# Kernel tuning notes

Hardware: AMD Instinct MI355X
Metric: run time of the kernel (lower is better)

Reference implementation:

```python
import jax, jax.numpy as jnp
import numpy as np

B = 64        # number of graphs
NPG = 4096    # nodes per graph (equal-size segments, batch ids sorted)
H = 256       # hidden_dim
C0, C1 = 256, 64  # num_clusters


def setup_inputs() -> dict:
    key = jax.random.key(0)
    ks = jax.random.split(key, 8)
    N = B * NPG
    x = jax.random.normal(ks[0], (N, H), dtype=jnp.float32)
    edge_index = jax.random.randint(ks[1], (2, N), 0, N, dtype=jnp.int64)  # unused by forward
    batch = jnp.repeat(jnp.arange(B, dtype=jnp.int64), NPG)  # sorted, equal-size segments
    s = 1.0 / np.sqrt(H)
    W0 = jax.random.uniform(ks[2], (H, C0), jnp.float32, -s, s)
    b0 = jax.random.uniform(ks[3], (C0,), jnp.float32, -s, s)
    W1 = jax.random.uniform(ks[4], (H, C1), jnp.float32, -s, s)
    b1 = jax.random.uniform(ks[5], (C1,), jnp.float32, -s, s)
    sf = 1.0 / np.sqrt(C1 * H)
    Wf = jax.random.uniform(ks[6], (C1 * H, H), jnp.float32, -sf, sf)
    bf = jax.random.uniform(ks[7], (H,), jnp.float32, -sf, sf)
    return {"x": x, "edge_index": edge_index, "batch": batch,
            "W0": W0, "b0": b0, "W1": W1, "b1": b1, "Wf": Wf, "bf": bf}


def reference(x, edge_index, batch, W0, b0, W1, b1, Wf, bf):
    # Level 0: softmax cluster assignment + per-graph segmented matmul A^T @ F.
    # batch ids are sorted with equal-size segments, so the per-graph Python
    # loop of the original collapses to a reshape + batched einsum.
    A0 = jax.nn.softmax(x @ W0 + b0, axis=-1)                      # [N, C0]
    f0 = jnp.einsum('bnc,bnh->bch',
                    A0.reshape(B, NPG, C0),
                    x.reshape(B, NPG, H)).reshape(B * C0, H)        # [B*C0, H]
    # Level 1: same pattern on pooled cluster features (C0 'nodes' per graph).
    A1 = jax.nn.softmax(f0 @ W1 + b1, axis=-1)                     # [B*C0, C1]
    f1 = jnp.einsum('bnc,bnh->bch',
                    A1.reshape(B, C0, C1),
                    f0.reshape(B, C0, H)).reshape(B, C1 * H)        # [B, C1*H]
    # Final pool: Linear -> ReLU (Dropout is identity in eval mode).
    return jax.nn.relu(f1 @ Wf + bf)                               # [B, H]
```

## Files before the change

kernel.cpp:

```cpp
#include <hip/hip_runtime.h>
#include <stdint.h>

#define NG   64
#define NPG  4096
#define HD   256
#define NC0  256
#define NC1  64
#define KSPLIT 2

typedef __attribute__((ext_vector_type(8))) short bfx8;
typedef __attribute__((ext_vector_type(4))) float fx4;

__device__ __forceinline__ unsigned short f2bf(float f) {
  union { float f; unsigned int u; } v; v.f = f;
  return (unsigned short)((v.u + 0x7FFFu + ((v.u >> 16) & 1u)) >> 16);
}
__device__ __forceinline__ unsigned int pack2(float a, float b) {
  return (unsigned int)f2bf(a) | ((unsigned int)f2bf(b) << 16);
}

#define ASYNC_COPY16(gptr, lptr) \
  __builtin_amdgcn_global_load_lds((const __attribute__((address_space(1))) unsigned int*)(gptr), \
                                   (__attribute__((address_space(3))) unsigned int*)(lptr), 16, 0, 0)

__global__ __launch_bounds__(256) void k_w0f(const float* __restrict__ W0,
                                             unsigned short* __restrict__ W0F) {
  int gid = blockIdx.x * 256 + threadIdx.x;
  int l15 = gid & 15;
  int q   = (gid >> 4) & 3;
  int ks  = (gid >> 6) & 1;
  int kc  = (gid >> 7) & 3;
  int cblk = gid >> 9;
  int c = cblk * 16 + l15;
  int kb = kc * 64 + ks * 32 + q * 8;
  unsigned int u[4];
  #pragma unroll
  for (int j = 0; j < 8; j += 2)
    u[j >> 1] = pack2(W0[(size_t)(kb + j) * 256 + c], W0[(size_t)(kb + j + 1) * 256 + c]);
  *(float4*)(W0F + (size_t)gid * 8) = *(float4*)u;
}

#define XSP 72
__global__ __launch_bounds__(512, 2) void k_assign0(
    const float* __restrict__ x, const unsigned short* __restrict__ W0F,
    const float* __restrict__ b0, unsigned short* __restrict__ A0T,
    unsigned short* __restrict__ xT, int g0) {
  __shared__ unsigned short xs[2][128 * XSP];
  __shared__ float red[128 * 4];
  unsigned short* at = (unsigned short*)xs;

  int gl = blockIdx.x >> 5, nt = blockIdx.x & 31;
  int tid = threadIdx.x;
  int wave = tid >> 6, lane = tid & 63;
  int wm = wave >> 2, wn = wave & 3;
  int l15 = lane & 15, q = lane >> 4;

  fx4 acc[4][4];
  #pragma unroll
  for (int i = 0; i < 4; ++i)
    #pragma unroll
    for (int j = 0; j < 4; ++j) acc[i][j] = fx4{0.f, 0.f, 0.f, 0.f};

  const float* xbase = x + ((size_t)(g0 + gl) * NPG + (size_t)nt * 128) * HD;
  int snode = tid >> 2, sseg = (tid & 3) * 16;

  {
    const float4* src = (const float4*)(xbase + (size_t)snode * HD + sseg);
    float4 v0 = src[0], v1 = src[1], v2 = src[2], v3 = src[3];
    float4 pv[2]; unsigned int* pu = (unsigned int*)pv;
    pu[0] = pack2(v0.x, v0.y); pu[1] = pack2(v0.z, v0.w);
    pu[2] = pack2(v1.x, v1.y); pu[3] = pack2(v1.z, v1.w);
    pu[4] = pack2(v2.x, v2.y); pu[5] = pack2(v2.z, v2.w);
    pu[6] = pack2(v3.x, v3.y); pu[7] = pack2(v3.z, v3.w);
    float4* d = (float4*)&xs[0][snode * XSP + sseg];
    d[0] = pv[0]; d[1] = pv[1];
  }
  __syncthreads();

  for (int kc = 0; kc < 4; ++kc) {
    int buf = kc & 1;
    if (kc < 3) {
      const float4* src = (const float4*)(xbase + (size_t)snode * HD + (kc + 1) * 64 + sseg);
      float4 v0 = src[0], v1 = src[1], v2 = src[2], v3 = src[3];
      float4 pv[2]; unsigned int* pu = (unsigned int*)pv;
      pu[0] = pack2(v0.x, v0.y); pu[1] = pack2(v0.z, v0.w);
      pu[2] = pack2(v1.x, v1.y); pu[3] = pack2(v1.z, v1.w);
      pu[4] = pack2(v2.x, v2.y); pu[5] = pack2(v2.z, v2.w);
      pu[6] = pack2(v3.x, v3.y); pu[7] = pack2(v3.z, v3.w);
      float4* d = (float4*)&xs[buf ^ 1][snode * XSP + sseg];
      d[0] = pv[0]; d[1] = pv[1];
    }
    #pragma unroll
    for (int ks = 0; ks < 2; ++ks) {
      int kk = ks * 32 + q * 8;
      bfx8 af[4];
      #pragma unroll
      for (int mi = 0; mi < 4; ++mi)
        af[mi] = *(const bfx8*)&xs[buf][(wm * 64 + mi * 16 + l15) * XSP + kk];
      #pragma unroll
      for (int ni = 0; ni < 4; ++ni) {
        bfx8 bv = *(const bfx8*)(W0F + ((size_t)(((wn * 4 + ni) * 8 + kc * 2 + ks) * 64 + lane)) * 8);
        #pragma unroll
        for (int mi = 0; mi < 4; ++mi)
          acc[mi][ni] = __builtin_amdgcn_mfma_f32_16x16x32_bf16(af[mi], bv, acc[mi][ni], 0, 0, 0);
      }
    }
    {
      int hl = tid >> 3;
      int seg = (tid & 7) * 16;
      unsigned int u[8];
      #pragma unroll
      for (int i = 0; i < 16; i += 2) {
        unsigned short a = xs[buf][(seg + i) * XSP + hl];
        unsigned short b = xs[buf][(seg + i + 1) * XSP + hl];
        u[i >> 1] = (unsigned int)a | ((unsigned int)b << 16);
      }
      float4* dst = (float4*)(xT + ((size_t)gl * HD + kc * 64 + hl) * NPG + (size_t)nt * 128 + seg);
      dst[0] = *(float4*)&u[0];
      dst[1] = *(float4*)&u[4];
    }
    __syncthreads();
  }

  float bv4[4];
  #pragma unroll
  for (int ni = 0; ni < 4; ++ni) bv4[ni] = b0[wn * 64 + ni * 16 + l15];
  #pragma unroll
  for (int mi = 0; mi < 4; ++mi)
    #pragma unroll
    for (int ni = 0; ni < 4; ++ni)
      #pragma unroll
      for (int r = 0; r < 4; ++r) acc[mi][ni][r] += bv4[ni];

  float mrow[4][4];
  #pragma unroll
  for (int mi = 0; mi < 4; ++mi)
    #pragma unroll
    for (int r = 0; r < 4; ++r) {
      float m = fmaxf(fmaxf(acc[mi][0][r], acc[mi][1][r]), fmaxf(acc[mi][2][r], acc[mi][3][r]));
      #pragma unroll
      for (int off = 1; off < 16; off <<= 1) m = fmaxf(m, __shfl_xor(m, off));
      mrow[mi][r] = m;
    }
  if (l15 == 0) {
    #pragma unroll
    for (int mi = 0; mi < 4; ++mi)
      #pragma unroll
      for (int r = 0; r < 4; ++r)
        red[(wm * 64 + mi * 16 + q * 4 + r) * 4 + wn] = mrow[mi][r];
  }
  __syncthreads();
  #pragma unroll
  for (int mi = 0; mi < 4; ++mi)
    #pragma unroll
    for (int r = 0; r < 4; ++r) {
      float4 rv = *(const float4*)&red[(wm * 64 + mi * 16 + q * 4 + r) * 4];
      mrow[mi][r] = fmaxf(fmaxf(rv.x, rv.y), fmaxf(rv.z, rv.w));
    }
  __syncthreads();
  float srow[4][4];
  #pragma unroll
  for (int mi = 0; mi < 4; ++mi)
    #pragma unroll
    for (int r = 0; r < 4; ++r) {
      float s = 0.f;
      #pragma unroll
      for (int ni = 0; ni < 4; ++ni) {
        float e = __expf(acc[mi][ni][r] - mrow[mi][r]);
        acc[mi][ni][r] = e; s += e;
      }
      #pragma unroll
      for (int off = 1; off < 16; off <<= 1) s += __shfl_xor(s, off);
      srow[mi][r] = s;
    }
  if (l15 == 0) {
    #pragma unroll
    for (int mi = 0; mi < 4; ++mi)
      #pragma unroll
      for (int r = 0; r < 4; ++r)
        red[(wm * 64 + mi * 16 + q * 4 + r) * 4 + wn] = srow[mi][r];
  }
  __syncthreads();
  #pragma unroll
  for (int mi = 0; mi < 4; ++mi)
    #pragma unroll
    for (int r = 0; r < 4; ++r) {
      float4 rv = *(const float4*)&red[(wm * 64 + mi * 16 + q * 4 + r) * 4];
      float inv = 1.f / (rv.x + rv.y + rv.z + rv.w);
      #pragma unroll
      for (int ni = 0; ni < 4; ++ni) acc[mi][ni][r] *= inv;
    }
  __syncthreads();

  unsigned short* A0Tg = A0T + (size_t)gl * NC0 * NPG + (size_t)nt * 128;
  #pragma unroll
  for (int p = 0; p < 2; ++p) {
    if ((wn >> 1) == p) {
      int cb = (wn & 1) * 64;
      #pragma unroll
      for (int mi = 0; mi < 4; ++mi) {
        int ncol = wm * 64 + mi * 16 + q * 4;
        #pragma unroll
        for (int ni = 0; ni < 4; ++ni) {
          int cl = cb + ni * 16 + l15;
          uint2 w;
          w.x = pack2(acc[mi][ni][0], acc[mi][ni][1]);
          w.y = pack2(acc[mi][ni][2], acc[mi][ni][3]);
          *(uint2*)(at + cl * 136 + ncol) = w;
        }
      }
    }
    __syncthreads();
    {
      int row = tid >> 2, seg = (tid & 3) * 32;
      const float4* s4 = (const float4*)(at + row * 136 + seg);
      float4 a = s4[0], b = s4[1], c = s4[2], d = s4[3];
      float4* d4 = (float4*)(A0Tg + (size_t)(p * 128 + row) * NPG + seg);
      d4[0] = a; d4[1] = b; d4[2] = c; d4[3] = d;
    }
    __syncthreads();
  }
}

__global__ __launch_bounds__(256, 2) void k_pool0(
    const unsigned short* __restrict__ A0T, const unsigned short* __restrict__ xT,
    float* __restrict__ f0p, int g0) {
  __shared__ unsigned short a_s[128 * 64];
  __shared__ unsigned short b_s[128 * 64];
  int bid = blockIdx.x;
  int kidx = bid & 1;
  int nt = (bid >> 1) & 1;
  int mt = (bid >> 2) & 1;
  int gl = bid >> 3;

  int tid = threadIdx.x;
  int wave = tid >> 6, lane = tid & 63;
  int wm = wave >> 1, wn = wave & 1;
  int l15 = lane & 15, q = lane >> 4;

  const int KPER = NPG / KSPLIT;
  const unsigned short* abase = A0T + ((size_t)gl * NC0 + (size_t)mt * 128) * NPG + (size_t)kidx * KPER;
  const unsigned short* bbase = xT  + ((size_t)gl * HD  + (size_t)nt * 128) * NPG + (size_t)kidx * KPER;

  fx4 acc[4][4];
  #pragma unroll
  for (int i = 0; i < 4; ++i)
    #pragma unroll
    for (int j = 0; j < 4; ++j) acc[i][j] = fx4{0.f, 0.f, 0.f, 0.f};

  int srow = lane >> 3;
  int sg   = (lane & 7) ^ srow;
  size_t soff = (size_t)srow * NPG + (size_t)sg * 8;

  for (int k0 = 0; k0 < KPER; k0 += 64) {
    #pragma unroll
    for (int i = 0; i < 4; ++i) {
      int r0 = wave * 32 + i * 8;
      ASYNC_COPY16(abase + (size_t)r0 * NPG + k0 + soff, &a_s[r0 * 64]);
      ASYNC_COPY16(bbase + (size_t)r0 * NPG + k0 + soff, &b_s[r0 * 64]);
    }
    __syncthreads();
    #pragma unroll
    for (int ks = 0; ks < 2; ++ks) {
      int gx = ((ks * 4 + q) ^ (l15 & 7)) << 3;
      bfx8 af[4], bf[4];
      #pragma unroll
      for (int mi = 0; mi < 4; ++mi)
        af[mi] = *(const bfx8*)&a_s[(wm * 64 + mi * 16 + l15) * 64 + gx];
      #pragma unroll
      for (int ni = 0; ni < 4; ++ni)
        bf[ni] = *(const bfx8*)&b_s[(wn * 64 + ni * 16 + l15) * 64 + gx];
      #pragma unroll
      for (int ni = 0; ni < 4; ++ni)
        #pragma unroll
        for (int mi = 0; mi < 4; ++mi)
          acc[mi][ni] = __builtin_amdgcn_mfma_f32_16x16x32_bf16(af[mi], bf[ni], acc[mi][ni], 0, 0, 0);
    }
    __syncthreads();
  }

  float* dst = f0p + (size_t)kidx * NG * NC0 * HD
             + ((size_t)(g0 + gl) * NC0 + (size_t)mt * 128) * HD + (size_t)nt * 128;
  #pragma unroll
  for (int mi = 0; mi < 4; ++mi)
    #pragma unroll
    for (int ni = 0; ni < 4; ++ni) {
      int c = wm * 64 + mi * 16 + q * 4;
      int h = wn * 64 + ni * 16 + l15;
      #pragma unroll
      for (int r = 0; r < 4; ++r)
        dst[(size_t)(c + r) * HD + h] = acc[mi][ni][r];
    }
}

__global__ __launch_bounds__(256) void k_f0sum(float* __restrict__ f0) {
  size_t i = ((size_t)blockIdx.x * 256 + threadIdx.x) * 4;
  float4 a = *(const float4*)(f0 + i);
  float4 b = *(const float4*)(f0 + (size_t)NG * NC0 * HD + i);
  a.x += b.x; a.y += b.y; a.z += b.z; a.w += b.w;
  *(float4*)(f0 + i) = a;
}

__global__ __launch_bounds__(256) void k_assign1(
    const float* __restrict__ f0, const float* __restrict__ W1,
    const float* __restrict__ b1, float* __restrict__ A1) {
  int row = blockIdx.x * 4 + (threadIdx.x >> 6);
  int lane = threadIdx.x & 63;
  const float* fr = f0 + (size_t)row * 256;
  float acc = b1[lane];
  for (int k = 0; k < 256; k += 4) {
    float4 fv = *(const float4*)(fr + k);
    acc += fv.x * W1[(k    ) * 64 + lane];
    acc += fv.y * W1[(k + 1) * 64 + lane];
    acc += fv.z * W1[(k + 2) * 64 + lane];
    acc += fv.w * W1[(k + 3) * 64 + lane];
  }
  float m = acc;
  #pragma unroll
  for (int off = 1; off < 64; off <<= 1) m = fmaxf(m, __shfl_xor(m, off));
  float e = __expf(acc - m);
  float s = e;
  #pragma unroll
  for (int off = 1; off < 64; off <<= 1) s += __shfl_xor(s, off);
  A1[(size_t)row * 64 + lane] = e / s;
}

__global__ __launch_bounds__(256) void k_pool1(
    const float* __restrict__ A1, const float* __restrict__ f0, float* __restrict__ f1) {
  int b = blockIdx.x >> 2, cg = blockIdx.x & 3;
  int h = threadIdx.x;
  const float* a1p = A1 + (size_t)b * NC0 * NC1 + cg * 16;
  const float* f0p = f0 + (size_t)b * NC0 * HD + h;
  float acc[16];
  #pragma unroll
  for (int j = 0; j < 16; ++j) acc[j] = 0.f;
  for (int c0 = 0; c0 < 256; ++c0) {
    float fv = f0p[(size_t)c0 * 256];
    #pragma unroll
    for (int j = 0; j < 16; ++j) acc[j] += a1p[c0 * 64 + j] * fv;
  }
  float* d = f1 + (size_t)b * 16384 + (size_t)(cg * 16) * 256 + h;
  #pragma unroll
  for (int j = 0; j < 16; ++j) d[(size_t)j * 256] = acc[j];
}

__global__ __launch_bounds__(256) void k_final_partial(
    const float* __restrict__ f1, const float* __restrict__ Wf, float* __restrict__ ot) {
  int b = blockIdx.x >> 4, kidx = blockIdx.x & 15;
  int h = threadIdx.x;
  const float* fp = f1 + (size_t)b * 16384 + (size_t)kidx * 1024;
  const float* wp = Wf + (size_t)kidx * 1024 * 256 + h;
  float acc = 0.f;
  for (int k = 0; k < 1024; k += 4) {
    float4 fv = *(const float4*)(fp + k);
    acc += fv.x * wp[(size_t)(k    ) * 256];
    acc += fv.y * wp[(size_t)(k + 1) * 256];
    acc += fv.z * wp[(size_t)(k + 2) * 256];
    acc += fv.w * wp[(size_t)(k + 3) * 256];
  }
  atomicAdd(&ot[b * 256 + h], acc);
}

__global__ __launch_bounds__(256) void k_final_out(
    const float* __restrict__ ot, const float* __restrict__ bfv, float* __restrict__ out) {
  int i = blockIdx.x * 256 + threadIdx.x;
  float v = ot[i] + bfv[i & 255];
  out[i] = v > 0.f ? v : 0.f;
}

extern "C" void kernel_launch(void* const* d_in, const int* in_sizes, int n_in,
                              void* d_out, int out_size, void* d_ws, size_t ws_size,
                              hipStream_t stream) {
  const float* x   = (const float*)d_in[0];
  const float* W0  = (const float*)d_in[3];
  const float* b0  = (const float*)d_in[4];
  const float* W1  = (const float*)d_in[5];
  const float* b1  = (const float*)d_in[6];
  const float* Wf  = (const float*)d_in[7];
  const float* bfv = (const float*)d_in[8];
  float* out = (float*)d_out;
  char* ws = (char*)d_ws;

  float* f0p = (float*)ws;
  float* f0  = f0p;
  float* ot  = (float*)(ws + ((size_t)32 << 20));
  unsigned short* W0F = (unsigned short*)(ws + ((size_t)32 << 20) + 65536);
  size_t chunk_off = ((size_t)32 << 20) + 65536 + 131072;
  size_t per_graph = (size_t)4 * HD * NPG;
  size_t avail = ws_size > chunk_off ? ws_size - chunk_off : 0;
  int G = (int)(avail / per_graph);
  if (G > 64) G = 64;
  if (G < 1) G = 1;
  unsigned short* xT  = (unsigned short*)(ws + chunk_off);
  unsigned short* A0T = xT + (size_t)G * HD * NPG;
  float* f1 = (float*)xT;
  float* A1 = (float*)A0T;

  hipMemsetAsync(ot, 0, 65536, stream);
  k_w0f<<<32, 256, 0, stream>>>(W0, W0F);

  for (int g0 = 0; g0 < NG; g0 += G) {
    int gc = (NG - g0 < G) ? (NG - g0) : G;
    k_assign0<<<gc * 32, 512, 0, stream>>>(x, W0F, b0, A0T, xT, g0);
    k_pool0<<<gc * 4 * KSPLIT, 256, 0, stream>>>(A0T, xT, f0p, g0);
  }
  k_f0sum<<<4096, 256, 0, stream>>>(f0);
  k_assign1<<<4096, 256, 0, stream>>>(f0, W1, b1, A1);
  k_pool1<<<256, 256, 0, stream>>>(A1, f0, f1);
  k_final_partial<<<64 * 16, 256, 0, stream>>>(f1, Wf, ot);
  k_final_out<<<64, 256, 0, stream>>>(ot, bfv, out);
}
```

Measured before the change: 751.8 us.

## Retile assign0 with swizzled LDS, stage W1 and f1 in shared memory

k_assign0 moves from 128-node tiles with 512 threads to 64-node tiles with 256 threads and four blocks per CU. Its LDS staging switches from padded rows to an XOR-swizzled layout, and the global loads are issued before the MFMA work so they overlap it. k_assign1 stages W1 in shared memory and computes 8 rows per wave, so W1 is no longer re-read from global memory for every row. k_final_partial stages a slice of f1 for all 64 graphs in LDS, so each Wf load serves 8 graphs, cutting Wf global traffic, at the cost of more atomics per block and fewer blocks.

```diff
diff --git a/kernel.cpp b/kernel.cpp
--- a/kernel.cpp
+++ b/kernel.cpp
@@ -40,19 +40,16 @@
   *(float4*)(W0F + (size_t)gid * 8) = *(float4*)u;
 }
 
-#define XSP 72
-__global__ __launch_bounds__(512, 2) void k_assign0(
+__global__ __launch_bounds__(256, 4) void k_assign0(
     const float* __restrict__ x, const unsigned short* __restrict__ W0F,
     const float* __restrict__ b0, unsigned short* __restrict__ A0T,
     unsigned short* __restrict__ xT, int g0) {
-  __shared__ unsigned short xs[2][128 * XSP];
-  __shared__ float red[128 * 4];
-  unsigned short* at = (unsigned short*)xs;
-
-  int gl = blockIdx.x >> 5, nt = blockIdx.x & 31;
+  __shared__ unsigned short lds_u[9216];
+  __shared__ float red[64 * 4];
+
+  int gl = blockIdx.x >> 6, nt = blockIdx.x & 63;
   int tid = threadIdx.x;
-  int wave = tid >> 6, lane = tid & 63;
-  int wm = wave >> 2, wn = wave & 3;
+  int wn = tid >> 6, lane = tid & 63;
   int l15 = lane & 15, q = lane >> 4;
 
   fx4 acc[4][4];
@@ -61,8 +58,10 @@
     #pragma unroll
     for (int j = 0; j < 4; ++j) acc[i][j] = fx4{0.f, 0.f, 0.f, 0.f};
 
-  const float* xbase = x + ((size_t)(g0 + gl) * NPG + (size_t)nt * 128) * HD;
+  const float* xbase = x + ((size_t)(g0 + gl) * NPG + (size_t)nt * 64) * HD;
   int snode = tid >> 2, sseg = (tid & 3) * 16;
+  int sg0  = sseg >> 3;
+  int sswz = (snode ^ (snode >> 4)) & 7;
 
   {
     const float4* src = (const float4*)(xbase + (size_t)snode * HD + sseg);
@@ -72,31 +71,28 @@
     pu[2] = pack2(v1.x, v1.y); pu[3] = pack2(v1.z, v1.w);
     pu[4] = pack2(v2.x, v2.y); pu[5] = pack2(v2.z, v2.w);
     pu[6] = pack2(v3.x, v3.y); pu[7] = pack2(v3.z, v3.w);
-    float4* d = (float4*)&xs[0][snode * XSP + sseg];
-    d[0] = pv[0]; d[1] = pv[1];
+    unsigned short* drow = &lds_u[snode << 6];
+    *(float4*)(drow + ((sg0 ^ sswz) << 3))       = pv[0];
+    *(float4*)(drow + (((sg0 + 1) ^ sswz) << 3)) = pv[1];
   }
   __syncthreads();
 
   for (int kc = 0; kc < 4; ++kc) {
     int buf = kc & 1;
+    const unsigned short* xb = &lds_u[buf * 4096];
+    float4 v0, v1, v2, v3;
     if (kc < 3) {
       const float4* src = (const float4*)(xbase + (size_t)snode * HD + (kc + 1) * 64 + sseg);
-      float4 v0 = src[0], v1 = src[1], v2 = src[2], v3 = src[3];
-      float4 pv[2]; unsigned int* pu = (unsigned int*)pv;
-      pu[0] = pack2(v0.x, v0.y); pu[1] = pack2(v0.z, v0.w);
-      pu[2] = pack2(v1.x, v1.y); pu[3] = pack2(v1.z, v1.w);
-      pu[4] = pack2(v2.x, v2.y); pu[5] = pack2(v2.z, v2.w);
-      pu[6] = pack2(v3.x, v3.y); pu[7] = pack2(v3.z, v3.w);
-      float4* d = (float4*)&xs[buf ^ 1][snode * XSP + sseg];
-      d[0] = pv[0]; d[1] = pv[1];
+      v0 = src[0]; v1 = src[1]; v2 = src[2]; v3 = src[3];
     }
     #pragma unroll
     for (int ks = 0; ks < 2; ++ks) {
-      int kk = ks * 32 + q * 8;
       bfx8 af[4];
       #pragma unroll
-      for (int mi = 0; mi < 4; ++mi)
-        af[mi] = *(const bfx8*)&xs[buf][(wm * 64 + mi * 16 + l15) * XSP + kk];
+      for (int mi = 0; mi < 4; ++mi) {
+        int slot = (ks * 4 + q) ^ (l15 & 7) ^ mi;
+        af[mi] = *(const bfx8*)&xb[((mi * 16 + l15) << 6) + (slot << 3)];
+      }
       #pragma unroll
       for (int ni = 0; ni < 4; ++ni) {
         bfx8 bv = *(const bfx8*)(W0F + ((size_t)(((wn * 4 + ni) * 8 + kc * 2 + ks) * 64 + lane)) * 8);
@@ -106,19 +102,30 @@
       }
     }
     {
-      int hl = tid >> 3;
-      int seg = (tid & 7) * 16;
+      int hl = tid >> 2, s4 = tid & 3, sg = s4 * 16;
+      int gcol = hl >> 3, off = hl & 7;
       unsigned int u[8];
       #pragma unroll
       for (int i = 0; i < 16; i += 2) {
-        unsigned short a = xs[buf][(seg + i) * XSP + hl];
-        unsigned short b = xs[buf][(seg + i + 1) * XSP + hl];
+        int r0 = sg + i;
+        unsigned short a = xb[(r0 << 6)       + ((gcol ^ (i & 7)       ^ s4) << 3) + off];
+        unsigned short b = xb[((r0 + 1) << 6) + ((gcol ^ ((i + 1) & 7) ^ s4) << 3) + off];
         u[i >> 1] = (unsigned int)a | ((unsigned int)b << 16);
       }
-      float4* dst = (float4*)(xT + ((size_t)gl * HD + kc * 64 + hl) * NPG + (size_t)nt * 128 + seg);
+      float4* dst = (float4*)(xT + ((size_t)gl * HD + kc * 64 + hl) * NPG + (size_t)nt * 64 + sg);
       dst[0] = *(float4*)&u[0];
       dst[1] = *(float4*)&u[4];
     }
+    if (kc < 3) {
+      float4 pv[2]; unsigned int* pu = (unsigned int*)pv;
+      pu[0] = pack2(v0.x, v0.y); pu[1] = pack2(v0.z, v0.w);
+      pu[2] = pack2(v1.x, v1.y); pu[3] = pack2(v1.z, v1.w);
+      pu[4] = pack2(v2.x, v2.y); pu[5] = pack2(v2.z, v2.w);
+      pu[6] = pack2(v3.x, v3.y); pu[7] = pack2(v3.z, v3.w);
+      unsigned short* drow = &lds_u[((buf ^ 1) * 4096) + (snode << 6)];
+      *(float4*)(drow + ((sg0 ^ sswz) << 3))       = pv[0];
+      *(float4*)(drow + (((sg0 + 1) ^ sswz) << 3)) = pv[1];
+    }
     __syncthreads();
   }
 
@@ -147,14 +154,14 @@
     for (int mi = 0; mi < 4; ++mi)
       #pragma unroll
       for (int r = 0; r < 4; ++r)
-        red[(wm * 64 + mi * 16 + q * 4 + r) * 4 + wn] = mrow[mi][r];
+        red[(mi * 16 + q * 4 + r) * 4 + wn] = mrow[mi][r];
   }
   __syncthreads();
   #pragma unroll
   for (int mi = 0; mi < 4; ++mi)
     #pragma unroll
     for (int r = 0; r < 4; ++r) {
-      float4 rv = *(const float4*)&red[(wm * 64 + mi * 16 + q * 4 + r) * 4];
+      float4 rv = *(const float4*)&red[(mi * 16 + q * 4 + r) * 4];
       mrow[mi][r] = fmaxf(fmaxf(rv.x, rv.y), fmaxf(rv.z, rv.w));
     }
   __syncthreads();
@@ -178,44 +185,45 @@
     for (int mi = 0; mi < 4; ++mi)
       #pragma unroll
       for (int r = 0; r < 4; ++r)
-        red[(wm * 64 + mi * 16 + q * 4 + r) * 4 + wn] = srow[mi][r];
+        red[(mi * 16 + q * 4 + r) * 4 + wn] = srow[mi][r];
   }
   __syncthreads();
   #pragma unroll
   for (int mi = 0; mi < 4; ++mi)
     #pragma unroll
     for (int r = 0; r < 4; ++r) {
-      float4 rv = *(const float4*)&red[(wm * 64 + mi * 16 + q * 4 + r) * 4];
+      float4 rv = *(const float4*)&red[(mi * 16 + q * 4 + r) * 4];
       float inv = 1.f / (rv.x + rv.y + rv.z + rv.w);
       #pragma unroll
       for (int ni = 0; ni < 4; ++ni) acc[mi][ni][r] *= inv;
     }
   __syncthreads();
 
-  unsigned short* A0Tg = A0T + (size_t)gl * NC0 * NPG + (size_t)nt * 128;
+  unsigned short* at = lds_u;
+  unsigned short* A0Tg = A0T + (size_t)gl * NC0 * NPG + (size_t)nt * 64;
   #pragma unroll
   for (int p = 0; p < 2; ++p) {
     if ((wn >> 1) == p) {
       int cb = (wn & 1) * 64;
       #pragma unroll
       for (int mi = 0; mi < 4; ++mi) {
-        int ncol = wm * 64 + mi * 16 + q * 4;
+        int ncol = mi * 16 + q * 4;
         #pragma unroll
         for (int ni = 0; ni < 4; ++ni) {
           int cl = cb + ni * 16 + l15;
           uint2 w;
           w.x = pack2(acc[mi][ni][0], acc[mi][ni][1]);
           w.y = pack2(acc[mi][ni][2], acc[mi][ni][3]);
-          *(uint2*)(at + cl * 136 + ncol) = w;
+          *(uint2*)(at + cl * 72 + ncol) = w;
         }
       }
     }
     __syncthreads();
     {
-      int row = tid >> 2, seg = (tid & 3) * 32;
-      const float4* s4 = (const float4*)(at + row * 136 + seg);
-      float4 a = s4[0], b = s4[1], c = s4[2], d = s4[3];
-      float4* d4 = (float4*)(A0Tg + (size_t)(p * 128 + row) * NPG + seg);
+      int row = tid >> 1, sg2 = (tid & 1) * 32;
+      const float4* s4p = (const float4*)(at + row * 72 + sg2);
+      float4 a = s4p[0], b = s4p[1], c = s4p[2], d = s4p[3];
+      float4* d4 = (float4*)(A0Tg + (size_t)(p * 128 + row) * NPG + sg2);
       d4[0] = a; d4[1] = b; d4[2] = c; d4[3] = d;
     }
     __syncthreads();
@@ -235,7 +243,7 @@
 
   int tid = threadIdx.x;
   int wave = tid >> 6, lane = tid & 63;
-  int wm = wave >> 1, wn = wave & 1;
+  int wm = wave >> 1, wnn = wave & 1;
   int l15 = lane & 15, q = lane >> 4;
 
   const int KPER = NPG / KSPLIT;
@@ -269,7 +277,7 @@
         af[mi] = *(const bfx8*)&a_s[(wm * 64 + mi * 16 + l15) * 64 + gx];
       #pragma unroll
       for (int ni = 0; ni < 4; ++ni)
-        bf[ni] = *(const bfx8*)&b_s[(wn * 64 + ni * 16 + l15) * 64 + gx];
+        bf[ni] = *(const bfx8*)&b_s[(wnn * 64 + ni * 16 + l15) * 64 + gx];
       #pragma unroll
       for (int ni = 0; ni < 4; ++ni)
         #pragma unroll
@@ -286,7 +294,7 @@
     #pragma unroll
     for (int ni = 0; ni < 4; ++ni) {
       int c = wm * 64 + mi * 16 + q * 4;
-      int h = wn * 64 + ni * 16 + l15;
+      int h = wnn * 64 + ni * 16 + l15;
       #pragma unroll
       for (int r = 0; r < 4; ++r)
         dst[(size_t)(c + r) * HD + h] = acc[mi][ni][r];
@@ -304,25 +312,37 @@
 __global__ __launch_bounds__(256) void k_assign1(
     const float* __restrict__ f0, const float* __restrict__ W1,
     const float* __restrict__ b1, float* __restrict__ A1) {
-  int row = blockIdx.x * 4 + (threadIdx.x >> 6);
-  int lane = threadIdx.x & 63;
-  const float* fr = f0 + (size_t)row * 256;
-  float acc = b1[lane];
-  for (int k = 0; k < 256; k += 4) {
-    float4 fv = *(const float4*)(fr + k);
-    acc += fv.x * W1[(k    ) * 64 + lane];
-    acc += fv.y * W1[(k + 1) * 64 + lane];
-    acc += fv.z * W1[(k + 2) * 64 + lane];
-    acc += fv.w * W1[(k + 3) * 64 + lane];
-  }
-  float m = acc;
-  #pragma unroll
-  for (int off = 1; off < 64; off <<= 1) m = fmaxf(m, __shfl_xor(m, off));
-  float e = __expf(acc - m);
-  float s = e;
-  #pragma unroll
-  for (int off = 1; off < 64; off <<= 1) s += __shfl_xor(s, off);
-  A1[(size_t)row * 64 + lane] = e / s;
+  __shared__ float w1s[256 * 64];
+  int tid = threadIdx.x;
+  #pragma unroll
+  for (int i = 0; i < 16; ++i) {
+    int off = i * 1024 + tid * 4;
+    *(float4*)(w1s + off) = *(const float4*)(W1 + off);
+  }
+  __syncthreads();
+  int lane = tid & 63;
+  int rbase = blockIdx.x * 32 + (tid >> 6) * 8;
+  float bias = b1[lane];
+  for (int rr = 0; rr < 8; ++rr) {
+    int row = rbase + rr;
+    const float* fr = f0 + (size_t)row * 256;
+    float acc = bias;
+    for (int k = 0; k < 256; k += 4) {
+      float4 fv = *(const float4*)(fr + k);
+      acc += fv.x * w1s[(k    ) * 64 + lane];
+      acc += fv.y * w1s[(k + 1) * 64 + lane];
+      acc += fv.z * w1s[(k + 2) * 64 + lane];
+      acc += fv.w * w1s[(k + 3) * 64 + lane];
+    }
+    float m = acc;
+    #pragma unroll
+    for (int off = 1; off < 64; off <<= 1) m = fmaxf(m, __shfl_xor(m, off));
+    float e = __expf(acc - m);
+    float s = e;
+    #pragma unroll
+    for (int off = 1; off < 64; off <<= 1) s += __shfl_xor(s, off);
+    A1[(size_t)row * 64 + lane] = e / s;
+  }
 }
 
 __global__ __launch_bounds__(256) void k_pool1(
@@ -344,21 +364,39 @@
   for (int j = 0; j < 16; ++j) d[(size_t)j * 256] = acc[j];
 }
 
-__global__ __launch_bounds__(256) void k_final_partial(
+__global__ __launch_bounds__(512) void k_final_partial(
     const float* __restrict__ f1, const float* __restrict__ Wf, float* __restrict__ ot) {
-  int b = blockIdx.x >> 4, kidx = blockIdx.x & 15;
-  int h = threadIdx.x;
-  const float* fp = f1 + (size_t)b * 16384 + (size_t)kidx * 1024;
-  const float* wp = Wf + (size_t)kidx * 1024 * 256 + h;
-  float acc = 0.f;
-  for (int k = 0; k < 1024; k += 4) {
-    float4 fv = *(const float4*)(fp + k);
-    acc += fv.x * wp[(size_t)(k    ) * 256];
-    acc += fv.y * wp[(size_t)(k + 1) * 256];
-    acc += fv.z * wp[(size_t)(k + 2) * 256];
-    acc += fv.w * wp[(size_t)(k + 3) * 256];
-  }
-  atomicAdd(&ot[b * 256 + h], acc);
+  __shared__ float f1s[64 * 256];
+  int ht = blockIdx.x & 3;
+  int ks = blockIdx.x >> 2;
+  int tid = threadIdx.x;
+  {
+    int b = tid >> 3, c0 = (tid & 7) * 4;
+    const float* s = f1 + (size_t)b * 16384 + (size_t)ks * 256 + c0;
+    float* d = f1s + b * 256 + c0;
+    #pragma unroll
+    for (int i = 0; i < 8; ++i) *(float4*)(d + i * 32) = *(const float4*)(s + i * 32);
+  }
+  __syncthreads();
+  int h = ht * 64 + (tid & 63);
+  int b0 = (tid >> 6) * 8;
+  const float* wp = Wf + (size_t)ks * 256 * 256 + h;
+  float acc[8];
+  #pragma unroll
+  for (int j = 0; j < 8; ++j) acc[j] = 0.f;
+  for (int k = 0; k < 256; k += 4) {
+    float w0 = wp[(size_t)(k    ) * 256];
+    float w1 = wp[(size_t)(k + 1) * 256];
+    float w2 = wp[(size_t)(k + 2) * 256];
+    float w3 = wp[(size_t)(k + 3) * 256];
+    #pragma unroll
+    for (int j = 0; j < 8; ++j) {
+      float4 fv = *(const float4*)(f1s + (b0 + j) * 256 + k);
+      acc[j] += fv.x * w0 + fv.y * w1 + fv.z * w2 + fv.w * w3;
+    }
+  }
+  #pragma unroll
+  for (int j = 0; j < 8; ++j) atomicAdd(&ot[(b0 + j) * 256 + h], acc[j]);
 }
 
 __global__ __launch_bounds__(256) void k_final_out(
@@ -401,12 +439,12 @@
 
   for (int g0 = 0; g0 < NG; g0 += G) {
     int gc = (NG - g0 < G) ? (NG - g0) : G;
-    k_assign0<<<gc * 32, 512, 0, stream>>>(x, W0F, b0, A0T, xT, g0);
+    k_assign0<<<gc * 64, 256, 0, stream>>>(x, W0F, b0, A0T, xT, g0);
     k_pool0<<<gc * 4 * KSPLIT, 256, 0, stream>>>(A0T, xT, f0p, g0);
   }
   k_f0sum<<<4096, 256, 0, stream>>>(f0);
-  k_assign1<<<4096, 256, 0, stream>>>(f0, W1, b1, A1);
+  k_assign1<<<512, 256, 0, stream>>>(f0, W1, b1, A1);
   k_pool1<<<256, 256, 0, stream>>>(A1, f0, f1);
-  k_final_partial<<<64 * 16, 256, 0, stream>>>(f1, Wf, ot);
+  k_final_partial<<<256, 512, 0, stream>>>(f1, Wf, ot);
   k_final_out<<<64, 256, 0, stream>>>(ot, bfv, out);
 }
```

Result: faster. 692.7 us (-7.9%).
